# Optimization experiments

Measured on AMD Instinct MI355X. Metric: run time of the kernel, lower is better.

Reference implementation:

```python
import jax, jax.numpy as jnp
import numpy as np

# dims
D = 1024      # d_model
DI = 2048     # d_inner = 2*d_model
N = 16        # d_state
RK = 64       # dt_rank
K = 4         # conv kernel
LYR = 15      # num_layers
BS = 64       # block_size
B = 4
L = 2048


def setup_inputs() -> dict:
    key = jax.random.key(0)
    ks = jax.random.split(key, 8)
    s = 0.02
    return {
        "x": jax.random.normal(ks[0], (B, L, D), jnp.float32),
        "norm_w": jnp.ones((LYR, D), jnp.float32),
        "in_proj_w": jax.random.normal(ks[1], (LYR, D, 2 * DI), jnp.float32) * s,
        "conv_w": jax.random.normal(ks[2], (LYR, K, DI), jnp.float32) * s,
        "conv_b": jnp.zeros((LYR, DI), jnp.float32),
        "x_dbc_w": jax.random.normal(ks[3], (LYR, DI, RK + 2 * N), jnp.float32) * s,
        "dt_w": jax.random.normal(ks[4], (LYR, RK, DI), jnp.float32) * s,
        "dt_b": jnp.zeros((LYR, DI), jnp.float32),
        "A_log": jnp.log(jnp.broadcast_to(jnp.arange(1, N + 1, dtype=jnp.float32), (LYR, DI, N))),
        "D_skip": jnp.ones((LYR, DI), jnp.float32),
        "out_proj_w": jax.random.normal(ks[5], (LYR, DI, D), jnp.float32) * s,
        "init_state": jnp.zeros((LYR, 1, 1, D), jnp.float32),
    }


def _rmsnorm(x, w, eps=1e-6):
    return x * jax.lax.rsqrt(jnp.mean(x * x, axis=-1, keepdims=True) + eps) * w


def _mamba_block(x, p):
    # x: (B, T1, D) with T1 = block_size + 1 (state token prepended)
    in_w, cw, cb, xdbc, dtw, dtb, Alog, Dsk, outw = p
    xz = jnp.einsum('btd,de->bte', x, in_w)
    xi, z = jnp.split(xz, 2, axis=-1)            # each (B, T1, DI)
    T1 = xi.shape[1]
    xp = jnp.pad(xi, ((0, 0), (K - 1, 0), (0, 0)))
    conv = sum(xp[:, i:i + T1, :] * cw[i] for i in range(K)) + cb  # causal depthwise conv
    u = jax.nn.silu(conv)
    dbc = jnp.einsum('bte,ef->btf', u, xdbc)
    dtr, Bc, Cc = jnp.split(dbc, [RK, RK + N], axis=-1)
    dt = jax.nn.softplus(jnp.einsum('btr,re->bte', dtr, dtw) + dtb)  # (B, T1, DI)
    A = -jnp.exp(Alog)                                                # (DI, N)

    def step(h, t):
        dt_t, u_t, B_t, C_t = t                                      # (B,DI),(B,DI),(B,N),(B,N)
        dA = jnp.exp(dt_t[..., None] * A)                            # (B, DI, N)
        h = dA * h + dt_t[..., None] * B_t[:, None, :] * u_t[..., None]
        y = jnp.einsum('ben,bn->be', h, C_t)
        return h, y

    h0 = jnp.zeros((x.shape[0], DI, N), x.dtype)
    xs = (dt.transpose(1, 0, 2), u.transpose(1, 0, 2),
          Bc.transpose(1, 0, 2), Cc.transpose(1, 0, 2))
    _, ys = jax.lax.scan(step, h0, xs)
    y = ys.transpose(1, 0, 2) + u * Dsk
    return jnp.einsum('bte,ed->btd', y * jax.nn.silu(z), outw)


def reference(x, norm_w, in_proj_w, conv_w, conv_b, x_dbc_w, dt_w, dt_b,
              A_log, D_skip, out_proj_w, init_state):
    Bsz, Lseq, Dm = x.shape
    nblocks = Lseq // BS
    chunks = x.reshape(Bsz, nblocks, BS, Dm).transpose(1, 0, 2, 3)   # (nb, B, BS, D)
    states0 = jnp.broadcast_to(init_state, (LYR, Bsz, 1, Dm))
    layer_params = (in_proj_w, conv_w, conv_b, x_dbc_w, dt_w, dt_b, A_log, D_skip, out_proj_w)

    def block_step(states, chunk):
        def layer_step(chunk_out, lp):
            nw, st = lp[0], lp[1]
            normed = _rmsnorm(chunk_out, nw)
            xin = jnp.concatenate([st, normed], axis=1)              # prepend state token
            lo = _mamba_block(xin, lp[2:])
            new_st = jax.lax.stop_gradient(lo[:, -1:, :])            # .detach()
            return chunk_out + lo[:, 1:, :], new_st

        chunk_out, new_states = jax.lax.scan(layer_step, chunk, (norm_w, states) + layer_params)
        return new_states, chunk_out

    _, outs = jax.lax.scan(block_step, states0, chunks)              # (nb, B, BS, D)
    return outs.transpose(1, 0, 2, 3).reshape(Bsz, Lseq, Dm)
```

## Files before the change

### kernel.cpp

```cpp
#include <hip/hip_runtime.h>

#define D_   1024
#define DI_  2048
#define NS_  16
#define RK_  64
#define KC_  4
#define LYR_ 15
#define BS_  64
#define B_   4
#define L_   2048
#define NB_  32
#define T1_  65
#define ROWS_ 260
#define PM_   384
#define XZW_ 4096
#define F_   96

typedef unsigned short u16;
typedef __attribute__((ext_vector_type(8))) short bf16x8;
typedef __attribute__((ext_vector_type(4))) float f32x4;

static __device__ __forceinline__ float bf2f(u16 u) {
  return __uint_as_float(((unsigned)u) << 16);
}
static __device__ __forceinline__ u16 f2bf(float f) {
  unsigned u = __float_as_uint(f);
  unsigned r = (u + 0x7fffu + ((u >> 16) & 1u)) >> 16;
  return (u16)r;
}
static __device__ __forceinline__ float ldf(const void* p, size_t i, int fp32) {
  return fp32 ? ((const float*)p)[i] : bf2f(((const u16*)p)[i]);
}
static __device__ __forceinline__ float fsilu(float x) { return x / (1.f + __expf(-x)); }
static __device__ __forceinline__ float fsoftplus(float x) {
  return x > 20.f ? x : log1pf(__expf(x));
}
static __device__ __forceinline__ void gload16(const void* g, void* l) {
  __builtin_amdgcn_global_load_lds(
      (const __attribute__((address_space(1))) void*)g,
      (__attribute__((address_space(3))) void*)l, 16, 0, 0);
}

__global__ void detect_k(const unsigned* __restrict__ nw_raw, int* __restrict__ flag) {
  if (blockIdx.x == 0 && threadIdx.x == 0)
    *flag = (nw_raw[0] == 0x3F800000u) ? 1 : 0;
}

__global__ void init_chunk(const void* __restrict__ x, float* __restrict__ chunk,
                           const int* __restrict__ flag, int ntot) {
  const int fp32 = *flag;
  int i = (blockIdx.x * 256 + threadIdx.x) * 4;
  if (i < ntot) {
    float4 o;
    if (fp32) {
      o = *(const float4*)((const float*)x + i);
    } else {
      ushort4 v = *(const ushort4*)((const u16*)x + i);
      o.x = bf2f(v.x); o.y = bf2f(v.y); o.z = bf2f(v.z); o.w = bf2f(v.w);
    }
    *(float4*)(chunk + i) = o;
  }
}

__global__ void init_states_k(const void* __restrict__ init_state,
                              float* __restrict__ states, const int* __restrict__ flag) {
  const int fp32 = *flag;
  int i = blockIdx.x * 256 + threadIdx.x;
  if (i < LYR_ * B_ * D_) {
    int l = i / (B_ * D_);
    int d = i & (D_ - 1);
    states[i] = ldf(init_state, (size_t)l * D_ + d, fp32);
  }
}

__global__ void zero4_k(float4* __restrict__ p, int n4) {
  int i = blockIdx.x * 256 + threadIdx.x;
  if (i < n4) { float4 z; z.x = z.y = z.z = z.w = 0.f; p[i] = z; }
}

__global__ void cvt_f32_k(const void* __restrict__ src, float* __restrict__ dst,
                          const int* __restrict__ flag, int n) {
  int i = blockIdx.x * 256 + threadIdx.x;
  if (i < n) dst[i] = ldf(src, i, *flag);
}

__global__ void cvt_aneg_k(const void* __restrict__ src, float* __restrict__ dst,
                           const int* __restrict__ flag, int n) {
  int i = blockIdx.x * 256 + threadIdx.x;
  if (i < n) dst[i] = -__expf(ldf(src, i, *flag));
}

__global__ __launch_bounds__(256) void transpose_bf16_k(
    const void* __restrict__ in, u16* __restrict__ out,
    const int* __restrict__ flag, int R, int C) {
  __shared__ float tile[32][33];
  const int fp32 = *flag;
  const int c0 = blockIdx.x * 32, r0 = blockIdx.y * 32;
  const size_t base = (size_t)blockIdx.z * R * C;
  const int tx = threadIdx.x & 31, ty = threadIdx.x >> 5;
  #pragma unroll
  for (int i = 0; i < 4; i++)
    tile[ty + i * 8][tx] = ldf(in, base + (size_t)(r0 + ty + i * 8) * C + c0 + tx, fp32);
  __syncthreads();
  #pragma unroll
  for (int i = 0; i < 4; i++)
    out[base + (size_t)(c0 + ty + i * 8) * R + r0 + tx] = f2bf(tile[tx][ty + i * 8]);
}

__global__ __launch_bounds__(256) void transpose_f32_k(
    const void* __restrict__ in, float* __restrict__ out,
    const int* __restrict__ flag, int R, int C) {
  __shared__ float tile[32][33];
  const int fp32 = *flag;
  const int c0 = blockIdx.x * 32, r0 = blockIdx.y * 32;
  const size_t base = (size_t)blockIdx.z * R * C;
  const int tx = threadIdx.x & 31, ty = threadIdx.x >> 5;
  #pragma unroll
  for (int i = 0; i < 4; i++)
    tile[ty + i * 8][tx] = ldf(in, base + (size_t)(r0 + ty + i * 8) * C + c0 + tx, fp32);
  __syncthreads();
  #pragma unroll
  for (int i = 0; i < 4; i++)
    out[base + (size_t)(c0 + ty + i * 8) * R + r0 + tx] = tile[tx][ty + i * 8];
}

__global__ __launch_bounds__(256) void prep_a_k(
    const float* __restrict__ chunk, const float* __restrict__ states,
    const float* __restrict__ nw_f, u16* __restrict__ apanel, int d, int lmin) {
  const int l = lmin + blockIdx.y;
  const int j = d - l;
  const int gr = blockIdx.x;
  const int tid = threadIdx.x;
  u16* out = apanel + ((size_t)l * PM_ + gr) * D_ + tid * 4;
  if (gr >= ROWS_) { *(ushort4*)out = make_ushort4(0, 0, 0, 0); return; }
  const int b = gr / T1_, t = gr - b * T1_;
  if (t == 0) {
    float4 v = *(const float4*)(states + ((size_t)l * B_ + b) * D_ + tid * 4);
    *(ushort4*)out = make_ushort4(f2bf(v.x), f2bf(v.y), f2bf(v.z), f2bf(v.w));
    return;
  }
  float4 v = *(const float4*)(chunk + ((size_t)b * L_ + (size_t)j * BS_ + (t - 1)) * D_ + tid * 4);
  float s = v.x * v.x + v.y * v.y + v.z * v.z + v.w * v.w;
  #pragma unroll
  for (int off = 32; off > 0; off >>= 1) s += __shfl_down(s, off);
  __shared__ float red[4];
  if ((tid & 63) == 0) red[tid >> 6] = s;
  __syncthreads();
  const float scale = rsqrtf((red[0] + red[1] + red[2] + red[3]) * (1.f / D_) + 1e-6f);
  float4 w = *(const float4*)(nw_f + (size_t)l * D_ + tid * 4);
  *(ushort4*)out = make_ushort4(f2bf(v.x * scale * w.x), f2bf(v.y * scale * w.y),
                                f2bf(v.z * scale * w.z), f2bf(v.w * scale * w.w));
}

__global__ __launch_bounds__(256) void gemm_in_k(
    const u16* __restrict__ apanel, const u16* __restrict__ winT,
    float* __restrict__ xi_all, u16* __restrict__ z_all, int lmin) {
  __shared__ __align__(16) u16 As[128 * 32];
  __shared__ __align__(16) u16 Bs[128 * 32];
  const int l = lmin + blockIdx.z;
  const int tid = threadIdx.x;
  const int m0 = blockIdx.y * 128;
  const int n0 = blockIdx.x * 128;
  const int lane = tid & 63, w = tid >> 6;
  const int wm = (w >> 1) * 64, wn = (w & 1) * 64;
  const int srow = tid >> 2, scol = (tid & 3) * 8;
  const u16* aG = apanel + ((size_t)l * PM_ + m0 + srow) * (size_t)D_ + scol;
  const u16* bG = winT + ((size_t)l * XZW_ + n0 + srow) * (size_t)D_ + scol;
  u16* aL = As + w * 512;
  u16* bL = Bs + w * 512;
  const int ar = lane & 15, kq = (lane >> 4) * 8;
  f32x4 acc[4][4];
  #pragma unroll
  for (int i = 0; i < 4; i++)
    #pragma unroll
    for (int jj = 0; jj < 4; jj++) acc[i][jj] = (f32x4){0.f, 0.f, 0.f, 0.f};
  for (int k0 = 0; k0 < D_; k0 += 32) {
    gload16(aG + k0, aL);
    gload16(aG + (size_t)64 * D_ + k0, aL + 2048);
    gload16(bG + k0, bL);
    gload16(bG + (size_t)64 * D_ + k0, bL + 2048);
    __syncthreads();
    bf16x8 av[4], bv[4];
    #pragma unroll
    for (int i = 0; i < 4; i++) av[i] = *(const bf16x8*)&As[(wm + i * 16 + ar) * 32 + kq];
    #pragma unroll
    for (int jj = 0; jj < 4; jj++) bv[jj] = *(const bf16x8*)&Bs[(wn + jj * 16 + ar) * 32 + kq];
    #pragma unroll
    for (int i = 0; i < 4; i++)
      #pragma unroll
      for (int jj = 0; jj < 4; jj++)
        acc[i][jj] = __builtin_amdgcn_mfma_f32_16x16x32_bf16(av[i], bv[jj], acc[i][jj], 0, 0, 0);
    __syncthreads();
  }
  const int rb = (lane >> 4) * 4, cb = lane & 15;
  if (n0 < DI_) {
    float* xi = xi_all + (size_t)l * ROWS_ * DI_;
    #pragma unroll
    for (int i = 0; i < 4; i++) {
      #pragma unroll
      for (int r = 0; r < 4; r++) {
        const int gr = m0 + wm + i * 16 + rb + r;
        if (gr < ROWS_) {
          #pragma unroll
          for (int jj = 0; jj < 4; jj++)
            xi[(size_t)gr * DI_ + n0 + wn + jj * 16 + cb] = acc[i][jj][r];
        }
      }
    }
  } else {
    u16* zb = z_all + (size_t)l * ROWS_ * DI_ + (n0 - DI_);
    #pragma unroll
    for (int i = 0; i < 4; i++) {
      #pragma unroll
      for (int r = 0; r < 4; r++) {
        const int gr = m0 + wm + i * 16 + rb + r;
        if (gr < ROWS_) {
          #pragma unroll
          for (int jj = 0; jj < 4; jj++)
            zb[(size_t)gr * DI_ + wn + jj * 16 + cb] = f2bf(acc[i][jj][r]);
        }
      }
    }
  }
}

__global__ __launch_bounds__(256) void conv_u_dbc_k(
    const float* __restrict__ xi_all, const float* __restrict__ convw_f,
    const float* __restrict__ convb_f, const float* __restrict__ xdbcT,
    float* __restrict__ u_all, float* __restrict__ dbcp_all, int lmin) {
  __shared__ float ut[16][132];
  __shared__ float xw[96][132];
  const int l = lmin + blockIdx.z;
  const int tid = threadIdx.x;
  const int r0 = blockIdx.y * 16, e0 = blockIdx.x * 128;
  {
    const int rr = tid >> 4, cc = (tid & 15) * 8;
    const float* xp = xdbcT + (size_t)l * F_ * DI_ + e0 + cc;
    #pragma unroll
    for (int it = 0; it < 6; it++) {
      int f = rr + it * 16;
      float4 w0 = *(const float4*)(xp + (size_t)f * DI_);
      float4 w1 = *(const float4*)(xp + (size_t)f * DI_ + 4);
      *(float4*)&xw[f][cc] = w0;
      *(float4*)&xw[f][cc + 4] = w1;
    }
  }
  {
    const int r = tid >> 4, eloc = (tid & 15) * 8;
    const int gr = r0 + r;
    if (gr < ROWS_) {
      const int b = gr / T1_, t = gr - b * T1_;
      const float* cbp = convb_f + (size_t)l * DI_ + e0 + eloc;
      float4 b0 = *(const float4*)cbp, b1 = *(const float4*)(cbp + 4);
      float a[8] = {b0.x, b0.y, b0.z, b0.w, b1.x, b1.y, b1.z, b1.w};
      const float* xi = xi_all + (size_t)l * ROWS_ * DI_;
      #pragma unroll
      for (int ki = 0; ki < KC_; ki++) {
        int tt = t - 3 + ki;
        if (tt >= 0) {
          const float* xp = xi + ((size_t)(b * T1_ + tt)) * DI_ + e0 + eloc;
          float4 x0 = *(const float4*)xp, x1 = *(const float4*)(xp + 4);
          const float* cwp = convw_f + ((size_t)l * KC_ + ki) * DI_ + e0 + eloc;
          float4 w0 = *(const float4*)cwp, w1 = *(const float4*)(cwp + 4);
          a[0] += x0.x * w0.x; a[1] += x0.y * w0.y; a[2] += x0.z * w0.z; a[3] += x0.w * w0.w;
          a[4] += x1.x * w1.x; a[5] += x1.y * w1.y; a[6] += x1.z * w1.z; a[7] += x1.w * w1.w;
        }
      }
      float4 s0, s1;
      s0.x = fsilu(a[0]); s0.y = fsilu(a[1]); s0.z = fsilu(a[2]); s0.w = fsilu(a[3]);
      s1.x = fsilu(a[4]); s1.y = fsilu(a[5]); s1.z = fsilu(a[6]); s1.w = fsilu(a[7]);
      float* up = u_all + (size_t)l * ROWS_ * DI_ + (size_t)gr * DI_ + e0 + eloc;
      *(float4*)up = s0; *(float4*)(up + 4) = s1;
      *(float4*)&ut[r][eloc] = s0; *(float4*)&ut[r][eloc + 4] = s1;
    } else {
      float4 z4 = {0, 0, 0, 0};
      *(float4*)&ut[r][eloc] = z4; *(float4*)&ut[r][eloc + 4] = z4;
    }
  }
  __syncthreads();
  {
    const int rr = tid >> 4, fg = tid & 15;
    const int gr = r0 + rr;
    float acc[6] = {0, 0, 0, 0, 0, 0};
    for (int k8 = 0; k8 < 16; k8++) {
      float4 u0 = *(const float4*)&ut[rr][k8 * 8];
      float4 u1 = *(const float4*)&ut[rr][k8 * 8 + 4];
      float uv[8] = {u0.x, u0.y, u0.z, u0.w, u1.x, u1.y, u1.z, u1.w};
      #pragma unroll
      for (int fi = 0; fi < 6; fi++) {
        const float* wp = &xw[fg + 16 * fi][k8 * 8];
        float4 w0 = *(const float4*)wp, w1 = *(const float4*)(wp + 4);
        acc[fi] += uv[0] * w0.x + uv[1] * w0.y + uv[2] * w0.z + uv[3] * w0.w
                 + uv[4] * w1.x + uv[5] * w1.y + uv[6] * w1.z + uv[7] * w1.w;
      }
    }
    if (gr < ROWS_) {
      float* dp = dbcp_all + (size_t)l * 16 * ROWS_ * F_ +
                  ((size_t)blockIdx.x * ROWS_ + gr) * F_;
      #pragma unroll
      for (int fi = 0; fi < 6; fi++) dp[fg + 16 * fi] = acc[fi];
    }
  }
}

__global__ __launch_bounds__(256) void dt_k(
    const float* __restrict__ dbcp_all, const float* __restrict__ dtw_f,
    const float* __restrict__ dtb_f, float* __restrict__ dt_all,
    float* __restrict__ bc_all, int lmin) {
  __shared__ float dtr_s[16][RK_];
  const int l = lmin + blockIdx.z;
  const int tid = threadIdx.x;
  const int r0 = blockIdx.y * 16, c0 = blockIdx.x * 256;
  const float* dbcp = dbcp_all + (size_t)l * 16 * ROWS_ * F_;
  #pragma unroll
  for (int q = 0; q < 4; q++) {
    int ii = tid * 4 + q;
    int rr = ii >> 6, cc = ii & 63;
    int gr = r0 + rr;
    float s = 0.f;
    if (gr < ROWS_) {
      #pragma unroll
      for (int p = 0; p < 16; p++) s += dbcp[((size_t)p * ROWS_ + gr) * F_ + cc];
    }
    dtr_s[rr][cc] = s;
  }
  if (blockIdx.x == 0) {
    #pragma unroll
    for (int q = 0; q < 2; q++) {
      int ii = tid * 2 + q;
      int rr = ii >> 5, cc = ii & 31;
      int gr = r0 + rr;
      if (gr < ROWS_) {
        float s = 0.f;
        #pragma unroll
        for (int p = 0; p < 16; p++) s += dbcp[((size_t)p * ROWS_ + gr) * F_ + RK_ + cc];
        bc_all[(size_t)l * ROWS_ * 32 + gr * 32 + cc] = s;
      }
    }
  }
  __syncthreads();
  const int rq = tid >> 6;
  const int col = c0 + (tid & 63) * 4;
  float acc[4][4];
  {
    float4 bv = *(const float4*)(dtb_f + (size_t)l * DI_ + col);
    float bb[4] = {bv.x, bv.y, bv.z, bv.w};
    #pragma unroll
    for (int r4 = 0; r4 < 4; r4++)
      #pragma unroll
      for (int c = 0; c < 4; c++) acc[r4][c] = bb[c];
  }
  const size_t wbase = (size_t)l * RK_ * DI_ + col;
  for (int k = 0; k < RK_; k++) {
    float4 wv4 = *(const float4*)(dtw_f + wbase + (size_t)k * DI_);
    float w[4] = {wv4.x, wv4.y, wv4.z, wv4.w};
    #pragma unroll
    for (int r4 = 0; r4 < 4; r4++) {
      float av = dtr_s[rq * 4 + r4][k];
      #pragma unroll
      for (int c = 0; c < 4; c++) acc[r4][c] += av * w[c];
    }
  }
  float* dtp = dt_all + (size_t)l * ROWS_ * DI_;
  #pragma unroll
  for (int r4 = 0; r4 < 4; r4++) {
    int gr = r0 + rq * 4 + r4;
    if (gr < ROWS_) {
      float4 o;
      o.x = fsoftplus(acc[r4][0]); o.y = fsoftplus(acc[r4][1]);
      o.z = fsoftplus(acc[r4][2]); o.w = fsoftplus(acc[r4][3]);
      *(float4*)(dtp + (size_t)gr * DI_ + col) = o;
    }
  }
}

__global__ __launch_bounds__(256) void scan_k(
    const float* __restrict__ dt_all, const float* __restrict__ u_all,
    const float* __restrict__ bc_all, const u16* __restrict__ z_all,
    const float* __restrict__ aneg_f, const float* __restrict__ dsk_f,
    u16* __restrict__ g_all, int lmin) {
  const int l = lmin + blockIdx.y;
  const int tid = threadIdx.x;
  const int b = blockIdx.x >> 3;
  const int e = ((blockIdx.x & 7) << 8) + tid;
  const float* dt = dt_all + (size_t)l * ROWS_ * DI_ + e;
  const float* uu = u_all  + (size_t)l * ROWS_ * DI_ + e;
  const float* bc = bc_all + (size_t)l * ROWS_ * 32;
  const u16*   zp = z_all  + (size_t)l * ROWS_ * DI_ + e;
  u16*         g  = g_all  + (size_t)l * PM_ * DI_ + e;
  float Av[16];
  {
    const float* ap = aneg_f + ((size_t)l * DI_ + e) * NS_;
    #pragma unroll
    for (int q = 0; q < 4; q++) {
      float4 a4 = *(const float4*)(ap + q * 4);
      Av[q * 4 + 0] = a4.x; Av[q * 4 + 1] = a4.y;
      Av[q * 4 + 2] = a4.z; Av[q * 4 + 3] = a4.w;
    }
  }
  const float Dv = dsk_f[(size_t)l * DI_ + e];
  float h[16];
  #pragma unroll
  for (int n = 0; n < 16; n++) h[n] = 0.f;
  for (int t = 0; t < T1_; t++) {
    const int row = b * T1_ + t;
    const float dtv = dt[(size_t)row * DI_];
    const float uv  = uu[(size_t)row * DI_];
    float4 b0 = *(const float4*)(bc + row * 32);
    float4 b1 = *(const float4*)(bc + row * 32 + 4);
    float4 b2 = *(const float4*)(bc + row * 32 + 8);
    float4 b3 = *(const float4*)(bc + row * 32 + 12);
    float4 c0 = *(const float4*)(bc + row * 32 + 16);
    float4 c1 = *(const float4*)(bc + row * 32 + 20);
    float4 c2 = *(const float4*)(bc + row * 32 + 24);
    float4 c3 = *(const float4*)(bc + row * 32 + 28);
    float bvv[16] = {b0.x, b0.y, b0.z, b0.w, b1.x, b1.y, b1.z, b1.w,
                     b2.x, b2.y, b2.z, b2.w, b3.x, b3.y, b3.z, b3.w};
    float cvv[16] = {c0.x, c0.y, c0.z, c0.w, c1.x, c1.y, c1.z, c1.w,
                     c2.x, c2.y, c2.z, c2.w, c3.x, c3.y, c3.z, c3.w};
    float p = 0.f;
    #pragma unroll
    for (int n = 0; n < 16; n++) {
      h[n] = __expf(dtv * Av[n]) * h[n] + (dtv * bvv[n]) * uv;
      p += h[n] * cvv[n];
    }
    const float z = bf2f(zp[(size_t)row * DI_]);
    g[(size_t)row * DI_] = f2bf((p + uv * Dv) * fsilu(z));
  }
}

__global__ __launch_bounds__(256) void gemm_out_k(
    const u16* __restrict__ g_all, const u16* __restrict__ woutT,
    float* __restrict__ chunk, void* __restrict__ dout,
    float* __restrict__ states, const int* __restrict__ flag, int d, int lmin) {
  __shared__ __align__(16) u16 Gs[128 * 32];
  __shared__ __align__(16) u16 Bs[64 * 32];
  const int l = lmin + blockIdx.z;
  const int j = d - l;
  const int last = (l == LYR_ - 1);
  const int fp32 = *flag;
  const int tid = threadIdx.x;
  const int m0 = blockIdx.y * 128;
  const int n0 = blockIdx.x * 64;
  const int lane = tid & 63, w = tid >> 6;
  const int wm = (w >> 1) * 64, wn = (w & 1) * 32;
  const int srow = tid >> 2, scol = (tid & 3) * 8;
  const u16* gG = g_all + ((size_t)l * PM_ + m0 + srow) * (size_t)DI_ + scol;
  const u16* bG = woutT + ((size_t)l * D_ + n0 + srow) * (size_t)DI_ + scol;
  u16* gL = Gs + w * 512;
  u16* bL = Bs + w * 512;
  const int ar = lane & 15, kq = (lane >> 4) * 8;
  f32x4 acc[4][2];
  #pragma unroll
  for (int i = 0; i < 4; i++)
    #pragma unroll
    for (int jj = 0; jj < 2; jj++) acc[i][jj] = (f32x4){0.f, 0.f, 0.f, 0.f};
  for (int k0 = 0; k0 < DI_; k0 += 32) {
    gload16(gG + k0, gL);
    gload16(gG + (size_t)64 * DI_ + k0, gL + 2048);
    gload16(bG + k0, bL);
    __syncthreads();
    bf16x8 av[4], bv[2];
    #pragma unroll
    for (int i = 0; i < 4; i++) av[i] = *(const bf16x8*)&Gs[(wm + i * 16 + ar) * 32 + kq];
    #pragma unroll
    for (int jj = 0; jj < 2; jj++) bv[jj] = *(const bf16x8*)&Bs[(wn + jj * 16 + ar) * 32 + kq];
    #pragma unroll
    for (int i = 0; i < 4; i++)
      #pragma unroll
      for (int jj = 0; jj < 2; jj++)
        acc[i][jj] = __builtin_amdgcn_mfma_f32_16x16x32_bf16(av[i], bv[jj], acc[i][jj], 0, 0, 0);
    __syncthreads();
  }
  const int rb = (lane >> 4) * 4, cb = lane & 15;
  #pragma unroll
  for (int i = 0; i < 4; i++) {
    #pragma unroll
    for (int r = 0; r < 4; r++) {
      const int gr = m0 + wm + i * 16 + rb + r;
      if (gr < ROWS_) {
        const int b = gr / T1_, t = gr - b * T1_;
        #pragma unroll
        for (int jj = 0; jj < 2; jj++) {
          const int dcol = n0 + wn + jj * 16 + cb;
          const float v = acc[i][jj][r];
          if (t == T1_ - 1) states[((size_t)l * B_ + b) * D_ + dcol] = v;
          if (t > 0) {
            const size_t off = ((size_t)b * L_ + (size_t)j * BS_ + (t - 1)) * D_ + dcol;
            const float nv = chunk[off] + v;
            chunk[off] = nv;
            if (last) {
              if (fp32) ((float*)dout)[off] = nv;
              else      ((u16*)dout)[off] = f2bf(nv);
            }
          }
        }
      }
    }
  }
}

extern "C" void kernel_launch(void* const* d_in, const int* in_sizes, int n_in,
                              void* d_out, int out_size, void* d_ws, size_t ws_size,
                              hipStream_t stream) {
  const void* x        = d_in[0];
  const void* norm_w   = d_in[1];
  const void* in_proj  = d_in[2];
  const void* conv_w   = d_in[3];
  const void* conv_b   = d_in[4];
  const void* xdbc_w   = d_in[5];
  const void* dt_w     = d_in[6];
  const void* dt_b     = d_in[7];
  const void* A_log    = d_in[8];
  const void* D_skip   = d_in[9];
  const void* out_proj = d_in[10];
  const void* init_st  = d_in[11];

  char* p = (char*)d_ws;
  auto carve = [&p](size_t bytes) -> char* {
    char* q = p;
    p += (bytes + 255) & ~((size_t)255);
    return q;
  };
  float* chunk   = (float*)carve((size_t)B_ * L_ * D_ * 4);
  u16*   winT    = (u16*)  carve((size_t)LYR_ * XZW_ * D_ * 2);
  u16*   woutT   = (u16*)  carve((size_t)LYR_ * D_ * DI_ * 2);
  float* xdbcT   = (float*)carve((size_t)LYR_ * F_ * DI_ * 4);
  float* convw_f = (float*)carve((size_t)LYR_ * KC_ * DI_ * 4);
  float* convb_f = (float*)carve((size_t)LYR_ * DI_ * 4);
  float* dtw_f   = (float*)carve((size_t)LYR_ * RK_ * DI_ * 4);
  float* dtb_f   = (float*)carve((size_t)LYR_ * DI_ * 4);
  float* aneg_f  = (float*)carve((size_t)LYR_ * DI_ * NS_ * 4);
  float* dsk_f   = (float*)carve((size_t)LYR_ * DI_ * 4);
  float* nw_f    = (float*)carve((size_t)LYR_ * D_ * 4);
  u16*   apanel  = (u16*)  carve((size_t)LYR_ * PM_ * D_ * 2);
  float* xi      = (float*)carve((size_t)LYR_ * ROWS_ * DI_ * 4);
  u16*   z_bf    = (u16*)  carve((size_t)LYR_ * ROWS_ * DI_ * 2);
  float* u       = (float*)carve((size_t)LYR_ * ROWS_ * DI_ * 4);
  float* dt      = (float*)carve((size_t)LYR_ * ROWS_ * DI_ * 4);
  float* dbcp    = (float*)carve((size_t)LYR_ * 16 * ROWS_ * F_ * 4);
  float* bc_cc   = (float*)carve((size_t)LYR_ * ROWS_ * 32 * 4);
  u16*   g_bf    = (u16*)  carve((size_t)LYR_ * PM_ * DI_ * 2);
  float* states  = (float*)carve((size_t)LYR_ * B_ * D_ * 4);
  int*   flag    = (int*)  carve(256);
  (void)in_sizes; (void)n_in; (void)out_size; (void)ws_size;

  detect_k<<<1, 64, 0, stream>>>((const unsigned*)norm_w, flag);
  init_chunk<<<(B_ * L_ * D_ / 4 + 255) / 256, 256, 0, stream>>>(x, chunk, flag, B_ * L_ * D_);
  init_states_k<<<(LYR_ * B_ * D_ + 255) / 256, 256, 0, stream>>>(init_st, states, flag);
  {
    int n4 = (int)((size_t)LYR_ * PM_ * DI_ * 2 / 16);
    zero4_k<<<(n4 + 255) / 256, 256, 0, stream>>>((float4*)g_bf, n4);
  }

  cvt_f32_k<<<(LYR_ * KC_ * DI_ + 255) / 256, 256, 0, stream>>>(conv_w, convw_f, flag, LYR_ * KC_ * DI_);
  cvt_f32_k<<<(LYR_ * DI_ + 255) / 256, 256, 0, stream>>>(conv_b, convb_f, flag, LYR_ * DI_);
  cvt_f32_k<<<(LYR_ * RK_ * DI_ + 255) / 256, 256, 0, stream>>>(dt_w, dtw_f, flag, LYR_ * RK_ * DI_);
  cvt_f32_k<<<(LYR_ * DI_ + 255) / 256, 256, 0, stream>>>(dt_b, dtb_f, flag, LYR_ * DI_);
  cvt_f32_k<<<(LYR_ * DI_ + 255) / 256, 256, 0, stream>>>(D_skip, dsk_f, flag, LYR_ * DI_);
  cvt_f32_k<<<(LYR_ * D_ + 255) / 256, 256, 0, stream>>>(norm_w, nw_f, flag, LYR_ * D_);
  cvt_aneg_k<<<(LYR_ * DI_ * NS_ + 255) / 256, 256, 0, stream>>>(A_log, aneg_f, flag, LYR_ * DI_ * NS_);
  transpose_bf16_k<<<dim3(XZW_ / 32, D_ / 32, LYR_), 256, 0, stream>>>(in_proj, winT, flag, D_, XZW_);
  transpose_bf16_k<<<dim3(D_ / 32, DI_ / 32, LYR_), 256, 0, stream>>>(out_proj, woutT, flag, DI_, D_);
  transpose_f32_k<<<dim3(F_ / 32, DI_ / 32, LYR_), 256, 0, stream>>>(xdbc_w, xdbcT, flag, DI_, F_);

  for (int dd = 0; dd < NB_ + LYR_ - 1; dd++) {
    int lmin = dd - (NB_ - 1); if (lmin < 0) lmin = 0;
    int lmax = dd < LYR_ - 1 ? dd : LYR_ - 1;
    int nc = lmax - lmin + 1;
    prep_a_k<<<dim3(PM_, nc), 256, 0, stream>>>(chunk, states, nw_f, apanel, dd, lmin);
    gemm_in_k<<<dim3(XZW_ / 128, PM_ / 128, nc), 256, 0, stream>>>(apanel, winT, xi, z_bf, lmin);
    conv_u_dbc_k<<<dim3(16, 17, nc), 256, 0, stream>>>(xi, convw_f, convb_f, xdbcT, u, dbcp, lmin);
    dt_k<<<dim3(8, 17, nc), 256, 0, stream>>>(dbcp, dtw_f, dtb_f, dt, bc_cc, lmin);
    scan_k<<<dim3(32, nc), 256, 0, stream>>>(dt, u, bc_cc, z_bf, aneg_f, dsk_f, g_bf, lmin);
    gemm_out_k<<<dim3(D_ / 64, PM_ / 128, nc), 256, 0, stream>>>(g_bf, woutT, chunk, d_out, states,
                                                                 flag, dd, lmin);
  }
}
```

Baseline: 13.40 ms.

## Split state-token rows out of GEMMs to shrink padded M from 384 to 256

Reorders rows so the 256 data rows (4 batches × 64 tokens) form the GEMM M dimension exactly, and the 4 state-token rows are handled separately. Their in-projection (xi half only) is computed by extra blocks in prep_a_k as a small matvec, and they are skipped in the out-projection GEMM since their output is never used. This removes a third of the MFMA tiles in both large GEMMs, drops the padding zero-fill kernel, and removes row-bound checks. The cost is a scalar dot-product path for the state rows and extra index remapping in the conv and scan kernels.

```diff
diff --git a/kernel.cpp b/kernel.cpp
--- a/kernel.cpp
+++ b/kernel.cpp
@@ -11,8 +11,8 @@
 #define L_   2048
 #define NB_  32
 #define T1_  65
-#define ROWS_ 260
-#define PM_   384
+#define NR_  260
+#define ND_  256
 #define XZW_ 4096
 #define F_   96
 
@@ -73,11 +73,6 @@
   }
 }
 
-__global__ void zero4_k(float4* __restrict__ p, int n4) {
-  int i = blockIdx.x * 256 + threadIdx.x;
-  if (i < n4) { float4 z; z.x = z.y = z.z = z.w = 0.f; p[i] = z; }
-}
-
 __global__ void cvt_f32_k(const void* __restrict__ src, float* __restrict__ dst,
                           const int* __restrict__ flag, int n) {
   int i = blockIdx.x * 256 + threadIdx.x;
@@ -126,30 +121,53 @@
 
 __global__ __launch_bounds__(256) void prep_a_k(
     const float* __restrict__ chunk, const float* __restrict__ states,
-    const float* __restrict__ nw_f, u16* __restrict__ apanel, int d, int lmin) {
+    const float* __restrict__ nw_f, u16* __restrict__ apanel,
+    const u16* __restrict__ winT, float* __restrict__ xi_all, int d, int lmin) {
+  __shared__ float red[4];
+  __shared__ float stl[1024][4];
   const int l = lmin + blockIdx.y;
-  const int j = d - l;
-  const int gr = blockIdx.x;
   const int tid = threadIdx.x;
-  u16* out = apanel + ((size_t)l * PM_ + gr) * D_ + tid * 4;
-  if (gr >= ROWS_) { *(ushort4*)out = make_ushort4(0, 0, 0, 0); return; }
-  const int b = gr / T1_, t = gr - b * T1_;
-  if (t == 0) {
-    float4 v = *(const float4*)(states + ((size_t)l * B_ + b) * D_ + tid * 4);
-    *(ushort4*)out = make_ushort4(f2bf(v.x), f2bf(v.y), f2bf(v.z), f2bf(v.w));
-    return;
-  }
-  float4 v = *(const float4*)(chunk + ((size_t)b * L_ + (size_t)j * BS_ + (t - 1)) * D_ + tid * 4);
-  float s = v.x * v.x + v.y * v.y + v.z * v.z + v.w * v.w;
-  #pragma unroll
-  for (int off = 32; off > 0; off >>= 1) s += __shfl_down(s, off);
-  __shared__ float red[4];
-  if ((tid & 63) == 0) red[tid >> 6] = s;
-  __syncthreads();
-  const float scale = rsqrtf((red[0] + red[1] + red[2] + red[3]) * (1.f / D_) + 1e-6f);
-  float4 w = *(const float4*)(nw_f + (size_t)l * D_ + tid * 4);
-  *(ushort4*)out = make_ushort4(f2bf(v.x * scale * w.x), f2bf(v.y * scale * w.y),
-                                f2bf(v.z * scale * w.z), f2bf(v.w * scale * w.w));
+  if (blockIdx.x < ND_) {
+    const int j = d - l;
+    const int gr = blockIdx.x;
+    const int b = gr >> 6, td = gr & 63;
+    float4 v = *(const float4*)(chunk + ((size_t)b * L_ + (size_t)j * BS_ + td) * D_ + tid * 4);
+    float s = v.x * v.x + v.y * v.y + v.z * v.z + v.w * v.w;
+    #pragma unroll
+    for (int off = 32; off > 0; off >>= 1) s += __shfl_down(s, off);
+    if ((tid & 63) == 0) red[tid >> 6] = s;
+    __syncthreads();
+    const float scale = rsqrtf((red[0] + red[1] + red[2] + red[3]) * (1.f / D_) + 1e-6f);
+    float4 w = *(const float4*)(nw_f + (size_t)l * D_ + tid * 4);
+    u16* out = apanel + ((size_t)l * ND_ + gr) * D_ + tid * 4;
+    *(ushort4*)out = make_ushort4(f2bf(v.x * scale * w.x), f2bf(v.y * scale * w.y),
+                                  f2bf(v.z * scale * w.z), f2bf(v.w * scale * w.w));
+  } else {
+    #pragma unroll
+    for (int q = 0; q < 16; q++) {
+      int idx = q * 256 + tid;
+      int k = idx >> 2, b = idx & 3;
+      stl[k][b] = bf2f(f2bf(states[((size_t)l * B_ + b) * D_ + k]));
+    }
+    __syncthreads();
+    const int col = (blockIdx.x - ND_) * 256 + tid;
+    const u16* wrow = winT + ((size_t)l * XZW_ + col) * (size_t)D_;
+    float a0 = 0.f, a1 = 0.f, a2 = 0.f, a3 = 0.f;
+    for (int k = 0; k < D_; k += 8) {
+      bf16x8 wv = *(const bf16x8*)(wrow + k);
+      #pragma unroll
+      for (int q = 0; q < 8; q++) {
+        float wf = bf2f((u16)wv[q]);
+        float4 sv = *(const float4*)&stl[k + q][0];
+        a0 += sv.x * wf; a1 += sv.y * wf; a2 += sv.z * wf; a3 += sv.w * wf;
+      }
+    }
+    float* xi = xi_all + (size_t)l * NR_ * DI_;
+    xi[(size_t)(ND_ + 0) * DI_ + col] = a0;
+    xi[(size_t)(ND_ + 1) * DI_ + col] = a1;
+    xi[(size_t)(ND_ + 2) * DI_ + col] = a2;
+    xi[(size_t)(ND_ + 3) * DI_ + col] = a3;
+  }
 }
 
 __global__ __launch_bounds__(256) void gemm_in_k(
@@ -164,7 +182,7 @@
   const int lane = tid & 63, w = tid >> 6;
   const int wm = (w >> 1) * 64, wn = (w & 1) * 64;
   const int srow = tid >> 2, scol = (tid & 3) * 8;
-  const u16* aG = apanel + ((size_t)l * PM_ + m0 + srow) * (size_t)D_ + scol;
+  const u16* aG = apanel + ((size_t)l * ND_ + m0 + srow) * (size_t)D_ + scol;
   const u16* bG = winT + ((size_t)l * XZW_ + n0 + srow) * (size_t)D_ + scol;
   u16* aL = As + w * 512;
   u16* bL = Bs + w * 512;
@@ -194,33 +212,27 @@
   }
   const int rb = (lane >> 4) * 4, cb = lane & 15;
   if (n0 < DI_) {
-    float* xi = xi_all + (size_t)l * ROWS_ * DI_;
-    #pragma unroll
-    for (int i = 0; i < 4; i++) {
+    float* xi = xi_all + (size_t)l * NR_ * DI_;
+    #pragma unroll
+    for (int i = 0; i < 4; i++)
       #pragma unroll
       for (int r = 0; r < 4; r++) {
         const int gr = m0 + wm + i * 16 + rb + r;
-        if (gr < ROWS_) {
-          #pragma unroll
-          for (int jj = 0; jj < 4; jj++)
-            xi[(size_t)gr * DI_ + n0 + wn + jj * 16 + cb] = acc[i][jj][r];
-        }
-      }
-    }
+        #pragma unroll
+        for (int jj = 0; jj < 4; jj++)
+          xi[(size_t)gr * DI_ + n0 + wn + jj * 16 + cb] = acc[i][jj][r];
+      }
   } else {
-    u16* zb = z_all + (size_t)l * ROWS_ * DI_ + (n0 - DI_);
-    #pragma unroll
-    for (int i = 0; i < 4; i++) {
+    u16* zb = z_all + (size_t)l * ND_ * DI_ + (n0 - DI_);
+    #pragma unroll
+    for (int i = 0; i < 4; i++)
       #pragma unroll
       for (int r = 0; r < 4; r++) {
         const int gr = m0 + wm + i * 16 + rb + r;
-        if (gr < ROWS_) {
-          #pragma unroll
-          for (int jj = 0; jj < 4; jj++)
-            zb[(size_t)gr * DI_ + wn + jj * 16 + cb] = f2bf(acc[i][jj][r]);
-        }
-      }
-    }
+        #pragma unroll
+        for (int jj = 0; jj < 4; jj++)
+          zb[(size_t)gr * DI_ + wn + jj * 16 + cb] = f2bf(acc[i][jj][r]);
+      }
   }
 }
 
@@ -248,17 +260,20 @@
   {
     const int r = tid >> 4, eloc = (tid & 15) * 8;
     const int gr = r0 + r;
-    if (gr < ROWS_) {
-      const int b = gr / T1_, t = gr - b * T1_;
+    if (gr < NR_) {
+      int b, t;
+      if (gr < ND_) { b = gr >> 6; t = (gr & 63) + 1; }
+      else          { b = gr - ND_; t = 0; }
       const float* cbp = convb_f + (size_t)l * DI_ + e0 + eloc;
       float4 b0 = *(const float4*)cbp, b1 = *(const float4*)(cbp + 4);
       float a[8] = {b0.x, b0.y, b0.z, b0.w, b1.x, b1.y, b1.z, b1.w};
-      const float* xi = xi_all + (size_t)l * ROWS_ * DI_;
+      const float* xi = xi_all + (size_t)l * NR_ * DI_;
       #pragma unroll
       for (int ki = 0; ki < KC_; ki++) {
         int tt = t - 3 + ki;
         if (tt >= 0) {
-          const float* xp = xi + ((size_t)(b * T1_ + tt)) * DI_ + e0 + eloc;
+          int rr2 = (tt == 0) ? ND_ + b : b * 64 + tt - 1;
+          const float* xp = xi + (size_t)rr2 * DI_ + e0 + eloc;
           float4 x0 = *(const float4*)xp, x1 = *(const float4*)(xp + 4);
           const float* cwp = convw_f + ((size_t)l * KC_ + ki) * DI_ + e0 + eloc;
           float4 w0 = *(const float4*)cwp, w1 = *(const float4*)(cwp + 4);
@@ -269,7 +284,7 @@
       float4 s0, s1;
       s0.x = fsilu(a[0]); s0.y = fsilu(a[1]); s0.z = fsilu(a[2]); s0.w = fsilu(a[3]);
       s1.x = fsilu(a[4]); s1.y = fsilu(a[5]); s1.z = fsilu(a[6]); s1.w = fsilu(a[7]);
-      float* up = u_all + (size_t)l * ROWS_ * DI_ + (size_t)gr * DI_ + e0 + eloc;
+      float* up = u_all + (size_t)l * NR_ * DI_ + (size_t)gr * DI_ + e0 + eloc;
       *(float4*)up = s0; *(float4*)(up + 4) = s1;
       *(float4*)&ut[r][eloc] = s0; *(float4*)&ut[r][eloc + 4] = s1;
     } else {
@@ -294,9 +309,9 @@
                  + uv[4] * w1.x + uv[5] * w1.y + uv[6] * w1.z + uv[7] * w1.w;
       }
     }
-    if (gr < ROWS_) {
-      float* dp = dbcp_all + (size_t)l * 16 * ROWS_ * F_ +
-                  ((size_t)blockIdx.x * ROWS_ + gr) * F_;
+    if (gr < NR_) {
+      float* dp = dbcp_all + (size_t)l * 16 * NR_ * F_ +
+                  ((size_t)blockIdx.x * NR_ + gr) * F_;
       #pragma unroll
       for (int fi = 0; fi < 6; fi++) dp[fg + 16 * fi] = acc[fi];
     }
@@ -311,16 +326,16 @@
   const int l = lmin + blockIdx.z;
   const int tid = threadIdx.x;
   const int r0 = blockIdx.y * 16, c0 = blockIdx.x * 256;
-  const float* dbcp = dbcp_all + (size_t)l * 16 * ROWS_ * F_;
+  const float* dbcp = dbcp_all + (size_t)l * 16 * NR_ * F_;
   #pragma unroll
   for (int q = 0; q < 4; q++) {
     int ii = tid * 4 + q;
     int rr = ii >> 6, cc = ii & 63;
     int gr = r0 + rr;
     float s = 0.f;
-    if (gr < ROWS_) {
-      #pragma unroll
-      for (int p = 0; p < 16; p++) s += dbcp[((size_t)p * ROWS_ + gr) * F_ + cc];
+    if (gr < NR_) {
+      #pragma unroll
+      for (int p = 0; p < 16; p++) s += dbcp[((size_t)p * NR_ + gr) * F_ + cc];
     }
     dtr_s[rr][cc] = s;
   }
@@ -330,11 +345,11 @@
       int ii = tid * 2 + q;
       int rr = ii >> 5, cc = ii & 31;
       int gr = r0 + rr;
-      if (gr < ROWS_) {
+      if (gr < NR_) {
         float s = 0.f;
         #pragma unroll
-        for (int p = 0; p < 16; p++) s += dbcp[((size_t)p * ROWS_ + gr) * F_ + RK_ + cc];
-        bc_all[(size_t)l * ROWS_ * 32 + gr * 32 + cc] = s;
+        for (int p = 0; p < 16; p++) s += dbcp[((size_t)p * NR_ + gr) * F_ + RK_ + cc];
+        bc_all[(size_t)l * NR_ * 32 + gr * 32 + cc] = s;
       }
     }
   }
@@ -361,11 +376,11 @@
       for (int c = 0; c < 4; c++) acc[r4][c] += av * w[c];
     }
   }
-  float* dtp = dt_all + (size_t)l * ROWS_ * DI_;
+  float* dtp = dt_all + (size_t)l * NR_ * DI_;
   #pragma unroll
   for (int r4 = 0; r4 < 4; r4++) {
     int gr = r0 + rq * 4 + r4;
-    if (gr < ROWS_) {
+    if (gr < NR_) {
       float4 o;
       o.x = fsoftplus(acc[r4][0]); o.y = fsoftplus(acc[r4][1]);
       o.z = fsoftplus(acc[r4][2]); o.w = fsoftplus(acc[r4][3]);
@@ -383,11 +398,11 @@
   const int tid = threadIdx.x;
   const int b = blockIdx.x >> 3;
   const int e = ((blockIdx.x & 7) << 8) + tid;
-  const float* dt = dt_all + (size_t)l * ROWS_ * DI_ + e;
-  const float* uu = u_all  + (size_t)l * ROWS_ * DI_ + e;
-  const float* bc = bc_all + (size_t)l * ROWS_ * 32;
-  const u16*   zp = z_all  + (size_t)l * ROWS_ * DI_ + e;
-  u16*         g  = g_all  + (size_t)l * PM_ * DI_ + e;
+  const float* dt = dt_all + (size_t)l * NR_ * DI_ + e;
+  const float* uu = u_all  + (size_t)l * NR_ * DI_ + e;
+  const float* bc = bc_all + (size_t)l * NR_ * 32;
+  const u16*   zp = z_all  + (size_t)l * ND_ * DI_ + e;
+  u16*         g  = g_all  + (size_t)l * ND_ * DI_ + e;
   float Av[16];
   {
     const float* ap = aneg_f + ((size_t)l * DI_ + e) * NS_;
@@ -402,8 +417,8 @@
   float h[16];
   #pragma unroll
   for (int n = 0; n < 16; n++) h[n] = 0.f;
-  for (int t = 0; t < T1_; t++) {
-    const int row = b * T1_ + t;
+  for (int t = 0; t <= 64; t++) {
+    const int row = (t == 0) ? ND_ + b : b * 64 + t - 1;
     const float dtv = dt[(size_t)row * DI_];
     const float uv  = uu[(size_t)row * DI_];
     float4 b0 = *(const float4*)(bc + row * 32);
@@ -424,8 +439,10 @@
       h[n] = __expf(dtv * Av[n]) * h[n] + (dtv * bvv[n]) * uv;
       p += h[n] * cvv[n];
     }
-    const float z = bf2f(zp[(size_t)row * DI_]);
-    g[(size_t)row * DI_] = f2bf((p + uv * Dv) * fsilu(z));
+    if (t > 0) {
+      const float z = bf2f(zp[(size_t)row * DI_]);
+      g[(size_t)row * DI_] = f2bf((p + uv * Dv) * fsilu(z));
+    }
   }
 }
 
@@ -445,7 +462,7 @@
   const int lane = tid & 63, w = tid >> 6;
   const int wm = (w >> 1) * 64, wn = (w & 1) * 32;
   const int srow = tid >> 2, scol = (tid & 3) * 8;
-  const u16* gG = g_all + ((size_t)l * PM_ + m0 + srow) * (size_t)DI_ + scol;
+  const u16* gG = g_all + ((size_t)l * ND_ + m0 + srow) * (size_t)DI_ + scol;
   const u16* bG = woutT + ((size_t)l * D_ + n0 + srow) * (size_t)DI_ + scol;
   u16* gL = Gs + w * 512;
   u16* bL = Bs + w * 512;
@@ -478,22 +495,18 @@
     #pragma unroll
     for (int r = 0; r < 4; r++) {
       const int gr = m0 + wm + i * 16 + rb + r;
-      if (gr < ROWS_) {
-        const int b = gr / T1_, t = gr - b * T1_;
-        #pragma unroll
-        for (int jj = 0; jj < 2; jj++) {
-          const int dcol = n0 + wn + jj * 16 + cb;
-          const float v = acc[i][jj][r];
-          if (t == T1_ - 1) states[((size_t)l * B_ + b) * D_ + dcol] = v;
-          if (t > 0) {
-            const size_t off = ((size_t)b * L_ + (size_t)j * BS_ + (t - 1)) * D_ + dcol;
-            const float nv = chunk[off] + v;
-            chunk[off] = nv;
-            if (last) {
-              if (fp32) ((float*)dout)[off] = nv;
-              else      ((u16*)dout)[off] = f2bf(nv);
-            }
-          }
+      const int b = gr >> 6, td = gr & 63;
+      #pragma unroll
+      for (int jj = 0; jj < 2; jj++) {
+        const int dcol = n0 + wn + jj * 16 + cb;
+        const float v = acc[i][jj][r];
+        if (td == 63) states[((size_t)l * B_ + b) * D_ + dcol] = v;
+        const size_t off = ((size_t)b * L_ + (size_t)j * BS_ + td) * D_ + dcol;
+        const float nv = chunk[off] + v;
+        chunk[off] = nv;
+        if (last) {
+          if (fp32) ((float*)dout)[off] = nv;
+          else      ((u16*)dout)[off] = f2bf(nv);
         }
       }
     }
@@ -533,14 +546,14 @@
   float* aneg_f  = (float*)carve((size_t)LYR_ * DI_ * NS_ * 4);
   float* dsk_f   = (float*)carve((size_t)LYR_ * DI_ * 4);
   float* nw_f    = (float*)carve((size_t)LYR_ * D_ * 4);
-  u16*   apanel  = (u16*)  carve((size_t)LYR_ * PM_ * D_ * 2);
-  float* xi      = (float*)carve((size_t)LYR_ * ROWS_ * DI_ * 4);
-  u16*   z_bf    = (u16*)  carve((size_t)LYR_ * ROWS_ * DI_ * 2);
-  float* u       = (float*)carve((size_t)LYR_ * ROWS_ * DI_ * 4);
-  float* dt      = (float*)carve((size_t)LYR_ * ROWS_ * DI_ * 4);
-  float* dbcp    = (float*)carve((size_t)LYR_ * 16 * ROWS_ * F_ * 4);
-  float* bc_cc   = (float*)carve((size_t)LYR_ * ROWS_ * 32 * 4);
-  u16*   g_bf    = (u16*)  carve((size_t)LYR_ * PM_ * DI_ * 2);
+  u16*   apanel  = (u16*)  carve((size_t)LYR_ * ND_ * D_ * 2);
+  float* xi      = (float*)carve((size_t)LYR_ * NR_ * DI_ * 4);
+  u16*   z_bf    = (u16*)  carve((size_t)LYR_ * ND_ * DI_ * 2);
+  float* u       = (float*)carve((size_t)LYR_ * NR_ * DI_ * 4);
+  float* dt      = (float*)carve((size_t)LYR_ * NR_ * DI_ * 4);
+  float* dbcp    = (float*)carve((size_t)LYR_ * 16 * NR_ * F_ * 4);
+  float* bc_cc   = (float*)carve((size_t)LYR_ * NR_ * 32 * 4);
+  u16*   g_bf    = (u16*)  carve((size_t)LYR_ * ND_ * DI_ * 2);
   float* states  = (float*)carve((size_t)LYR_ * B_ * D_ * 4);
   int*   flag    = (int*)  carve(256);
   (void)in_sizes; (void)n_in; (void)out_size; (void)ws_size;
@@ -548,10 +561,6 @@
   detect_k<<<1, 64, 0, stream>>>((const unsigned*)norm_w, flag);
   init_chunk<<<(B_ * L_ * D_ / 4 + 255) / 256, 256, 0, stream>>>(x, chunk, flag, B_ * L_ * D_);
   init_states_k<<<(LYR_ * B_ * D_ + 255) / 256, 256, 0, stream>>>(init_st, states, flag);
-  {
-    int n4 = (int)((size_t)LYR_ * PM_ * DI_ * 2 / 16);
-    zero4_k<<<(n4 + 255) / 256, 256, 0, stream>>>((float4*)g_bf, n4);
-  }
 
   cvt_f32_k<<<(LYR_ * KC_ * DI_ + 255) / 256, 256, 0, stream>>>(conv_w, convw_f, flag, LYR_ * KC_ * DI_);
   cvt_f32_k<<<(LYR_ * DI_ + 255) / 256, 256, 0, stream>>>(conv_b, convb_f, flag, LYR_ * DI_);
@@ -568,12 +577,12 @@
     int lmin = dd - (NB_ - 1); if (lmin < 0) lmin = 0;
     int lmax = dd < LYR_ - 1 ? dd : LYR_ - 1;
     int nc = lmax - lmin + 1;
-    prep_a_k<<<dim3(PM_, nc), 256, 0, stream>>>(chunk, states, nw_f, apanel, dd, lmin);
-    gemm_in_k<<<dim3(XZW_ / 128, PM_ / 128, nc), 256, 0, stream>>>(apanel, winT, xi, z_bf, lmin);
+    prep_a_k<<<dim3(ND_ + 8, nc), 256, 0, stream>>>(chunk, states, nw_f, apanel, winT, xi, dd, lmin);
+    gemm_in_k<<<dim3(XZW_ / 128, 2, nc), 256, 0, stream>>>(apanel, winT, xi, z_bf, lmin);
     conv_u_dbc_k<<<dim3(16, 17, nc), 256, 0, stream>>>(xi, convw_f, convb_f, xdbcT, u, dbcp, lmin);
     dt_k<<<dim3(8, 17, nc), 256, 0, stream>>>(dbcp, dtw_f, dtb_f, dt, bc_cc, lmin);
     scan_k<<<dim3(32, nc), 256, 0, stream>>>(dt, u, bc_cc, z_bf, aneg_f, dsk_f, g_bf, lmin);
-    gemm_out_k<<<dim3(D_ / 64, PM_ / 128, nc), 256, 0, stream>>>(g_bf, woutT, chunk, d_out, states,
-                                                                 flag, dd, lmin);
-  }
-}
+    gemm_out_k<<<dim3(D_ / 64, 2, nc), 256, 0, stream>>>(g_bf, woutT, chunk, d_out, states,
+                                                         flag, dd, lmin);
+  }
+}
```

New measurement: 14.18 ms. 1.06x slower.
